# Optimization experiments

Hardware: AMD Instinct MI355X
Metric: run time of the kernel (lower is better)

## Reference

```python
import jax, jax.numpy as jnp
import numpy as np

B, S, D, F, E, CAP = 4, 2048, 1024, 4096, 8, 320


def setup_inputs() -> dict:
    key = jax.random.key(0)
    k1, k2, k3, k4 = jax.random.split(key, 4)
    return {
        "hidden_states": jax.random.normal(k1, (B, S, D), dtype=jnp.float32),
        "router_w": jax.random.normal(k2, (D, E), dtype=jnp.float32) * 0.02,
        "wi": jax.random.normal(k3, (E, D, F), dtype=jnp.float32) * 0.02,
        "wo": jax.random.normal(k4, (E, F, D), dtype=jnp.float32) * 0.02,
    }


def reference(hidden_states, router_w, wi, wo):
    # ---- Router (Switch top-1 with per-sequence expert capacity) ----
    b, s, d = hidden_states.shape
    e = router_w.shape[1]
    logits = hidden_states.astype(jnp.float32) @ router_w          # [B,S,E]
    probs = jax.nn.softmax(logits, axis=-1)                        # [B,S,E]
    expert_idx = jnp.argmax(probs, axis=-1)                        # [B,S]
    onehot = jax.nn.one_hot(expert_idx, e, dtype=jnp.int32)        # [B,S,E]
    priority = jnp.cumsum(onehot, axis=1)                          # cumsum over seq dim (dim=-2)
    keep = onehot * (priority <= CAP).astype(jnp.int32)            # capacity-masked router_mask

    # slot of each token within its chosen expert (0-based)
    slot = jnp.take_along_axis(priority, expert_idx[..., None], axis=-1)[..., 0] - 1  # [B,S]
    valid = slot < CAP                                             # dropped tokens exceed capacity
    slot_sc = jnp.where(valid, slot, CAP)                          # out-of-range -> dropped by scatter

    b_ar = jnp.broadcast_to(jnp.arange(b)[:, None], (b, s))
    s_ar = jnp.broadcast_to(jnp.arange(s)[None, :], (b, s))
    dispatch = jnp.zeros((b, e, CAP), jnp.int32).at[b_ar, expert_idx, slot_sc].set(
        s_ar.astype(jnp.int32), mode="drop")                       # [B,E,CAP] token index per slot
    slot_used = jnp.zeros((b, e, CAP), bool).at[b_ar, expert_idx, slot_sc].set(
        valid, mode="drop")                                        # [B,E,CAP]

    # ---- Dispatch: gather tokens into [B,E,CAP,D] ----
    xg = jax.vmap(lambda xb, ib: xb[ib])(hidden_states, dispatch)  # [B,E,CAP,D]

    # ---- Per-expert dense FFN (grouped GEMM) ----
    hg = jax.nn.relu(jnp.einsum("becd,edf->becf", xg, wi))         # [B,E,CAP,F]
    yg = jnp.einsum("becf,efd->becd", hg, wo)                      # [B,E,CAP,D]

    # ---- Combine: scatter expert outputs back; unrouted tokens keep input ----
    idx_back = jnp.where(slot_used, dispatch, s)                   # out-of-range -> dropped
    next_states = jax.vmap(
        lambda xb, ib, yb: xb.at[ib.reshape(-1)].set(yb.reshape(-1, d), mode="drop")
    )(hidden_states, idx_back, yg)                                 # [B,S,D]

    max_prob = jnp.max(probs, axis=-1, keepdims=True)              # [B,S,1]
    out = max_prob * next_states
    expert_index_out = jnp.argmax(keep, axis=-1)                   # [B,S] (0 for dropped tokens)
    return out, logits, expert_index_out
```

## Files before the change

kernel.cpp:

```cpp
#include <hip/hip_runtime.h>
#include <hip/hip_bf16.h>
#include <stdint.h>

#define B_ 4
#define S_ 2048
#define D_ 1024
#define F_ 4096
#define E_ 8
#define CAP_ 320
#define BS_ (B_*S_)
#define MPE 1280

typedef unsigned short u16;
typedef __attribute__((ext_vector_type(8))) short bf16x8;
typedef __attribute__((ext_vector_type(4))) float f32x4;
typedef __attribute__((ext_vector_type(4))) unsigned short u16x4;

__device__ __forceinline__ u16 f2bf(float f) {
  union { float f; uint32_t u; } v; v.f = f;
  uint32_t r = (v.u + 0x7FFFu + ((v.u >> 16) & 1u)) >> 16;
  return (u16)r;
}

__device__ __forceinline__ void gload16(const void* g, void* l) {
  __builtin_amdgcn_global_load_lds(
      (const __attribute__((address_space(1))) uint32_t*)g,
      (__attribute__((address_space(3))) uint32_t*)l, 16, 0, 0);
}

__global__ __launch_bounds__(256) void router_kernel(
    const float* __restrict__ hs, const float* __restrict__ rw,
    float* __restrict__ out, float* __restrict__ logits,
    float* __restrict__ maxp, int* __restrict__ eidx)
{
  const int wv = threadIdx.x >> 6, l = threadIdx.x & 63;
  const int token = blockIdx.x * 4 + wv;
  const float* row = hs + (size_t)token * D_;
  const float4* rw4 = (const float4*)rw;

  double acc0=0, acc1=0, acc2=0, acc3=0, acc4=0, acc5=0, acc6=0, acc7=0;
  float4 v[4];
#pragma unroll
  for (int j = 0; j < 4; ++j) {
    const int d4 = l + j * 64;
    v[j] = ((const float4*)row)[d4];
#pragma unroll
    for (int c = 0; c < 4; ++c) {
      const int d = d4 * 4 + c;
      const float x = (&v[j].x)[c];
      const float4 w0 = rw4[d * 2];
      const float4 w1 = rw4[d * 2 + 1];
      acc0 += (double)x * (double)w0.x;
      acc1 += (double)x * (double)w0.y;
      acc2 += (double)x * (double)w0.z;
      acc3 += (double)x * (double)w0.w;
      acc4 += (double)x * (double)w1.x;
      acc5 += (double)x * (double)w1.y;
      acc6 += (double)x * (double)w1.z;
      acc7 += (double)x * (double)w1.w;
    }
  }
  double acc[E_] = {acc0, acc1, acc2, acc3, acc4, acc5, acc6, acc7};
#pragma unroll
  for (int e = 0; e < E_; ++e) {
#pragma unroll
    for (int off = 32; off; off >>= 1)
      acc[e] += __shfl_xor(acc[e], off);
  }
  float lg[E_];
#pragma unroll
  for (int e = 0; e < E_; ++e) lg[e] = (float)acc[e];

  float lmax = lg[0]; int am = 0;
#pragma unroll
  for (int e = 1; e < E_; ++e) { if (lg[e] > lmax) { lmax = lg[e]; am = e; } }
  float sum = 0.f;
#pragma unroll
  for (int e = 0; e < E_; ++e) sum += expf(lg[e] - lmax);
  const float mp = 1.0f / sum;

  float* orow = out + (size_t)token * D_;
#pragma unroll
  for (int j = 0; j < 4; ++j) {
    float4 o;
    o.x = v[j].x * mp; o.y = v[j].y * mp; o.z = v[j].z * mp; o.w = v[j].w * mp;
    ((float4*)orow)[l + j * 64] = o;
  }
  if (l == 0) {
#pragma unroll
    for (int e = 0; e < E_; ++e) logits[(size_t)token * E_ + e] = lg[e];
    maxp[token] = mp;
    eidx[token] = am;
  }
}

__global__ __launch_bounds__(256) void scan_kernel(
    const int* __restrict__ eidx, int* __restrict__ tok,
    float* __restrict__ eout)
{
  const int b = blockIdx.x >> 3, e = blockIdx.x & 7;
  __shared__ int wsum[4];
  const int tid = threadIdx.x, wv = tid >> 6, l = tid & 63;
  int base = 0;
  for (int ch = 0; ch < S_ / 256; ++ch) {
    const int s = ch * 256 + tid;
    const bool p = (eidx[b * S_ + s] == e);
    const unsigned long long m = __ballot(p);
    const int lp = __popcll(m & ((1ULL << l) - 1ULL));
    if (l == 0) wsum[wv] = __popcll(m);
    __syncthreads();
    int pre = 0, tot = 0;
#pragma unroll
    for (int w = 0; w < 4; ++w) { if (w < wv) pre += wsum[w]; tot += wsum[w]; }
    if (p) {
      const int rank = base + pre + lp;
      if (rank < CAP_) tok[(b * E_ + e) * CAP_ + rank] = s;
      eout[b * S_ + s] = (rank < CAP_) ? (float)e : 0.0f;
    }
    base += tot;
    __syncthreads();
  }
}

__global__ __launch_bounds__(256) void transpose_kernel(
    const float* __restrict__ W, u16* __restrict__ WT, int K, int N)
{
  __shared__ float tile[32][33];
  const int tiles_k = K >> 5, tiles_n = N >> 5;
  const int e = blockIdx.x / (tiles_k * tiles_n);
  const int r = blockIdx.x % (tiles_k * tiles_n);
  const int k0 = (r / tiles_n) << 5, n0 = (r % tiles_n) << 5;
  const int tx = threadIdx.x & 31, ty = threadIdx.x >> 5;
  const float* We = W + (size_t)e * K * N;
  u16* WTe = WT + (size_t)e * K * N;
#pragma unroll
  for (int i = 0; i < 4; ++i)
    tile[ty + i * 8][tx] = We[(size_t)(k0 + ty + i * 8) * N + (n0 + tx)];
  __syncthreads();
#pragma unroll
  for (int i = 0; i < 4; ++i) {
    const int n = n0 + ty + i * 8, k = k0 + tx;
    WTe[(size_t)n * K + k] = f2bf(tile[tx][ty + i * 8]);
  }
}

__global__ __launch_bounds__(256) void gather_kernel(
    const float* __restrict__ hs, const int* __restrict__ tok,
    u16* __restrict__ Xg)
{
  const int bx = blockIdx.x;
  const int e = bx / MPE, r = bx % MPE;
  const int b = r / CAP_, c = r % CAP_;
  const int t = tok[(b * E_ + e) * CAP_ + c];
  const int d = threadIdx.x * 4;
  u16x4 o;
  if (t >= 0) {
    const float4 vv = *(const float4*)(hs + ((size_t)(b * S_ + t)) * D_ + d);
    o[0] = f2bf(vv.x); o[1] = f2bf(vv.y); o[2] = f2bf(vv.z); o[3] = f2bf(vv.w);
  } else {
    o[0] = 0; o[1] = 0; o[2] = 0; o[3] = 0;
  }
  *(u16x4*)(Xg + (size_t)bx * D_ + d) = o;
}

template<int MODE>
__global__ __launch_bounds__(512, 2) void moe_gemm8(
    const u16* __restrict__ Aall, const u16* __restrict__ Btall,
    u16* __restrict__ hgout, float* __restrict__ out,
    const int* __restrict__ tok, const float* __restrict__ maxp,
    const int K, const int ntn)
{
  __shared__ __align__(16) u16 lds[2][2][2][8192];

  const int nwg = gridDim.x;
  const int cpx = nwg >> 3;
  const int bid = blockIdx.x;
  const int swzb = (bid & 7) * cpx + (bid >> 3);
  const int bpe = 5 * ntn;
  const int e = swzb / bpe, rem = swzb % bpe;
  const int m0 = (rem / ntn) * 256, n0 = (rem % ntn) * 256;
  const int N = ntn * 256;

  const u16* Ae = Aall + (size_t)e * MPE * K;
  const u16* Be = Btall + (size_t)e * N * K;

  const int tid = threadIdx.x;
  const int wv = tid >> 6, l = tid & 63;
  const int wr = wv >> 2, wc = wv & 3;
  const int lr = l & 15, lk = l >> 4;
  const int rswz = ((lr >> 3) & 1) << 4;
  const int gs0 = tid ^ (((tid >> 5) & 1) << 1);
  const size_t goff = (size_t)((gs0 >> 2) & 127) * K + (size_t)((gs0 & 3) * 8);
  const int dwoff = wv * 512;

  const u16* pA0 = Ae + (size_t)m0 * K;
  const u16* pA1 = Ae + (size_t)(m0 + 128) * K;
  const u16* pB0 = Be + (size_t)n0 * K;
  const u16* pB1 = Be + (size_t)(n0 + 128) * K;

  const int NT = K >> 6;

  f32x4 acc[8][4];
#pragma unroll
  for (int i = 0; i < 8; ++i)
#pragma unroll
    for (int j = 0; j < 4; ++j) acc[i][j] = (f32x4){0.f, 0.f, 0.f, 0.f};

  bf16x8 fa[8], fb0[4], fb1[4];

#define LDSH(p, ab, h) (&lds[p][ab][h][0])

#define STAGE(dhalf, rb, tt) do {                                          \
    const u16* s_ = (rb) + goff + (size_t)((tt) * 64);                     \
    gload16(s_,      (dhalf) + dwoff);                                     \
    gload16(s_ + 32, (dhalf) + 4096 + dwoff);                              \
  } while (0)

#define READ_A(msub, p) do {                                               \
    _Pragma("unroll")                                                      \
    for (int mf = 0; mf < 4; ++mf)                                         \
      _Pragma("unroll")                                                    \
      for (int kk = 0; kk < 2; ++kk)                                       \
        fa[mf*2+kk] = *(const bf16x8*)&lds[p][0][wr]                       \
            [(kk*128 + (msub)*64 + mf*16 + lr)*32 + ((lk*8) ^ rswz)];      \
  } while (0)

#define READ_B(nsub, p, fb) do {                                           \
    _Pragma("unroll")                                                      \
    for (int nf = 0; nf < 2; ++nf)                                         \
      _Pragma("unroll")                                                    \
      for (int kk = 0; kk < 2; ++kk)                                       \
        fb[nf*2+kk] = *(const bf16x8*)&lds[p][1][wc>>1]                    \
            [(kk*128 + (wc&1)*64 + (nsub)*32 + nf*16 + lr)*32              \
             + ((lk*8) ^ rswz)];                                           \
  } while (0)

#define MFMA_Q(msub, nsub, fb) do {                                        \
    __builtin_amdgcn_s_setprio(1);                                         \
    _Pragma("unroll")                                                      \
    for (int mf = 0; mf < 4; ++mf)                                         \
      _Pragma("unroll")                                                    \
      for (int nf = 0; nf < 2; ++nf)                                       \
        _Pragma("unroll")                                                  \
        for (int kk = 0; kk < 2; ++kk)                                     \
          acc[(msub)*4+mf][(nsub)*2+nf] =                                  \
              __builtin_amdgcn_mfma_f32_16x16x32_bf16(                     \
                  fa[mf*2+kk], fb[nf*2+kk],                                \
                  acc[(msub)*4+mf][(nsub)*2+nf], 0, 0, 0);                 \
    __builtin_amdgcn_s_setprio(0);                                         \
  } while (0)

#define BAR() __builtin_amdgcn_s_barrier()
#define LGKM0() do { asm volatile("s_waitcnt lgkmcnt(0)" ::: "memory");    \
                     __builtin_amdgcn_sched_barrier(0); } while (0)
#define VM4() asm volatile("s_waitcnt vmcnt(4)" ::: "memory")

#define DO_TILE(p, pn, tA, tB) do {                                        \
                                                                   \
    READ_A(0, p); READ_B(0, p, fb0);                                       \
    STAGE(LDSH(pn, 0, 0), pA0, (tA));                                      \
    BAR(); LGKM0();                                                        \
    MFMA_Q(0, 0, fb0);                                                     \
    BAR();                                                                 \
                                                                   \
    READ_B(1, p, fb1);                                                     \
    STAGE(LDSH(pn, 0, 1), pA1, (tA));                                      \
    BAR(); LGKM0();                                                        \
    MFMA_Q(0, 1, fb1);                                                     \
    BAR();                                                                 \
                                                                   \
    READ_A(1, p);                                                          \
    STAGE(LDSH(p, 1, 0), pB0, (tB));                                       \
    BAR(); LGKM0();                                                        \
    MFMA_Q(1, 0, fb0);                                                     \
    BAR();                                                                 \
                                                                   \
    STAGE(LDSH(p, 1, 1), pB1, (tB));                                       \
    BAR();                                                                 \
    MFMA_Q(1, 1, fb1);                                                     \
    VM4(); BAR();                                                          \
  } while (0)

  STAGE(LDSH(0, 1, 0), pB0, 0);
  STAGE(LDSH(0, 1, 1), pB1, 0);
  STAGE(LDSH(0, 0, 0), pA0, 0);
  STAGE(LDSH(0, 0, 1), pA1, 0);
  STAGE(LDSH(1, 1, 0), pB0, 1);
  STAGE(LDSH(1, 1, 1), pB1, 1);
  VM4(); BAR();

  for (int t = 0; t < NT; t += 2) {
    const int tB0 = (t + 2 < NT) ? t + 2 : t;
    const int tB1 = (t + 3 < NT) ? t + 3 : t + 1;
    DO_TILE(0, 1, t + 1, tB0);
    DO_TILE(1, 0, tB0, tB1);
  }

  if (MODE == 1) {
#pragma unroll
    for (int i = 0; i < 8; ++i) {
#pragma unroll
      for (int r = 0; r < 4; ++r) {
        const int grow = m0 + wr * 128 + i * 16 + lk * 4 + r;
        u16* hrow = hgout + ((size_t)e * MPE + grow) * (size_t)N + n0 + wc * 64;
#pragma unroll
        for (int j = 0; j < 4; ++j)
          hrow[j * 16 + lr] = f2bf(fmaxf(acc[i][j][r], 0.0f));
      }
    }
  } else {
#pragma unroll
    for (int i = 0; i < 8; ++i) {
#pragma unroll
      for (int r = 0; r < 4; ++r) {
        const int grow = m0 + wr * 128 + i * 16 + lk * 4 + r;
        const int b = grow / CAP_, c = grow % CAP_;
        const int t = tok[(b * E_ + e) * CAP_ + c];
        if (t >= 0) {
          const float sc = maxp[b * S_ + t];
          float* orow = out + ((size_t)(b * S_ + t)) * D_ + n0 + wc * 64;
#pragma unroll
          for (int j = 0; j < 4; ++j)
            orow[j * 16 + lr] = sc * acc[i][j][r];
        }
      }
    }
  }
#undef LDSH
#undef STAGE
#undef READ_A
#undef READ_B
#undef MFMA_Q
#undef BAR
#undef LGKM0
#undef VM4
#undef DO_TILE
}

extern "C" void kernel_launch(void* const* d_in, const int* in_sizes, int n_in,
                              void* d_out, int out_size, void* d_ws, size_t ws_size,
                              hipStream_t stream)
{
  const float* hs = (const float*)d_in[0];
  const float* rw = (const float*)d_in[1];
  const float* wi = (const float*)d_in[2];
  const float* wo = (const float*)d_in[3];

  float* out    = (float*)d_out;
  float* logits = out + (size_t)BS_ * D_;
  float* eout   = logits + (size_t)BS_ * E_;

  uint8_t* ws = (uint8_t*)d_ws;
  int*   tok  = (int*)(ws + 0);
  float* maxp = (float*)(ws + 40960);
  int*   eidx = (int*)(ws + 73728);
  u16*   Xg   = (u16*)(ws + 131072);
  u16*   hg   = (u16*)(ws + 21102592);
  u16*   wT   = (u16*)(ws + 104988672);
  if (ws_size < 172097536ULL) return;

  hipMemsetAsync(tok, 0xFF, 40960, stream);

  router_kernel<<<BS_ / 4, 256, 0, stream>>>(hs, rw, out, logits, maxp, eidx);
  scan_kernel<<<B_ * E_, 256, 0, stream>>>(eidx, tok, eout);
  transpose_kernel<<<E_ * (D_ / 32) * (F_ / 32), 256, 0, stream>>>(wi, wT, D_, F_);
  gather_kernel<<<E_ * MPE, 256, 0, stream>>>(hs, tok, Xg);
  moe_gemm8<1><<<E_ * 5 * (F_ / 256), 512, 0, stream>>>(
      Xg, wT, hg, nullptr, tok, maxp, D_, F_ / 256);
  transpose_kernel<<<E_ * (F_ / 32) * (D_ / 32), 256, 0, stream>>>(wo, wT, F_, D_);
  moe_gemm8<2><<<E_ * 5 * (D_ / 256), 512, 0, stream>>>(
      hg, wT, nullptr, out, tok, maxp, F_, D_ / 256);
}
```

Before: 340.3 us.

## Fuse weight transposes into router and GEMM launches, restructure GEMM prefetch pipeline

The wi transpose is merged into the router launch as extra blocks, and when workspace allows, the wo transpose is appended as extra blocks to the first GEMM launch. The transpose is rewritten with bigger 128x64 tiles and 16-byte bf16 stores. The per-token scaling of unrouted outputs moves from the router into the scan, so only dropped tokens are copied, and the memset is replaced by in-kernel initialisation. The GEMM K-loop prefetch order and vmcnt waits are reworked to stage A further ahead. The goal is fewer launches, better transpose bandwidth and overlap, at the cost of more complex scheduling and extra LDS use in the fused paths.

```diff
diff --git a/kernel.cpp b/kernel.cpp
--- a/kernel.cpp
+++ b/kernel.cpp
@@ -15,6 +15,7 @@
 typedef __attribute__((ext_vector_type(8))) short bf16x8;
 typedef __attribute__((ext_vector_type(4))) float f32x4;
 typedef __attribute__((ext_vector_type(4))) unsigned short u16x4;
+typedef __attribute__((ext_vector_type(8))) unsigned short u16x8;
 
 __device__ __forceinline__ u16 f2bf(float f) {
   union { float f; uint32_t u; } v; v.f = f;
@@ -28,26 +29,68 @@
       (__attribute__((address_space(3))) uint32_t*)l, 16, 0, 0);
 }
 
-__global__ __launch_bounds__(256) void router_kernel(
+__device__ __forceinline__ void transpose_block(
+    const float* __restrict__ W, u16* __restrict__ WT,
+    const int K, const int N, const int bid, void* ldsraw)
+{
+  float (*tile)[65] = (float(*)[65])ldsraw;
+  const int tk = K >> 7, tn = N >> 6;
+  const int e = bid / (tk * tn), r = bid % (tk * tn);
+  const int k0 = (r / tn) << 7, n0 = (r % tn) << 6;
+  const float* We = W + (size_t)e * K * N;
+  u16* WTe = WT + (size_t)e * N * K;
+  const int t = threadIdx.x;
+  const int fr = t >> 2, c0 = (t & 3) * 16;
+#pragma unroll
+  for (int j = 0; j < 4; ++j) {
+    const float4 v = *(const float4*)(We + (size_t)(k0 + fr) * N + n0 + c0 + j * 4);
+    tile[fr][c0 + j*4 + 0] = v.x; tile[fr][c0 + j*4 + 1] = v.y;
+    tile[fr][c0 + j*4 + 2] = v.z; tile[fr][c0 + j*4 + 3] = v.w;
+  }
+  __syncthreads();
+  const int nr = t >> 3, kk0 = (t & 7) * 16;
+  u16x8 o0, o1;
+#pragma unroll
+  for (int j = 0; j < 8; ++j) o0[j] = f2bf(tile[kk0 + j][nr]);
+#pragma unroll
+  for (int j = 0; j < 8; ++j) o1[j] = f2bf(tile[kk0 + 8 + j][nr]);
+  u16* dst = WTe + (size_t)(n0 + nr) * K + k0 + kk0;
+  *(u16x8*)dst = o0;
+  *(u16x8*)(dst + 8) = o1;
+}
+
+__global__ __launch_bounds__(512) void transpose_kernel(
+    const float* __restrict__ W, u16* __restrict__ WT, const int K, const int N)
+{
+  __shared__ __align__(16) float tile[128][65];
+  transpose_block(W, WT, K, N, blockIdx.x, (void*)tile);
+}
+
+__global__ __launch_bounds__(512) void prep_kernel(
     const float* __restrict__ hs, const float* __restrict__ rw,
-    float* __restrict__ out, float* __restrict__ logits,
-    float* __restrict__ maxp, int* __restrict__ eidx)
-{
+    const float* __restrict__ wi, u16* __restrict__ wT,
+    float* __restrict__ logits, float* __restrict__ maxp,
+    int* __restrict__ eidx, const int twiT)
+{
+  __shared__ __align__(16) float tile[128][65];
+  if ((int)blockIdx.x < twiT) {
+    transpose_block(wi, wT, D_, F_, blockIdx.x, (void*)tile);
+    return;
+  }
   const int wv = threadIdx.x >> 6, l = threadIdx.x & 63;
-  const int token = blockIdx.x * 4 + wv;
+  const int token = (blockIdx.x - twiT) * 8 + wv;
   const float* row = hs + (size_t)token * D_;
   const float4* rw4 = (const float4*)rw;
 
   double acc0=0, acc1=0, acc2=0, acc3=0, acc4=0, acc5=0, acc6=0, acc7=0;
-  float4 v[4];
 #pragma unroll
   for (int j = 0; j < 4; ++j) {
     const int d4 = l + j * 64;
-    v[j] = ((const float4*)row)[d4];
+    const float4 v = ((const float4*)row)[d4];
 #pragma unroll
     for (int c = 0; c < 4; ++c) {
       const int d = d4 * 4 + c;
-      const float x = (&v[j].x)[c];
+      const float x = (&v.x)[c];
       const float4 w0 = rw4[d * 2];
       const float4 w1 = rw4[d * 2 + 1];
       acc0 += (double)x * (double)w0.x;
@@ -67,40 +110,33 @@
     for (int off = 32; off; off >>= 1)
       acc[e] += __shfl_xor(acc[e], off);
   }
-  float lg[E_];
-#pragma unroll
-  for (int e = 0; e < E_; ++e) lg[e] = (float)acc[e];
-
-  float lmax = lg[0]; int am = 0;
-#pragma unroll
-  for (int e = 1; e < E_; ++e) { if (lg[e] > lmax) { lmax = lg[e]; am = e; } }
-  float sum = 0.f;
-#pragma unroll
-  for (int e = 0; e < E_; ++e) sum += expf(lg[e] - lmax);
-  const float mp = 1.0f / sum;
-
-  float* orow = out + (size_t)token * D_;
-#pragma unroll
-  for (int j = 0; j < 4; ++j) {
-    float4 o;
-    o.x = v[j].x * mp; o.y = v[j].y * mp; o.z = v[j].z * mp; o.w = v[j].w * mp;
-    ((float4*)orow)[l + j * 64] = o;
-  }
   if (l == 0) {
+    float lg[E_];
+#pragma unroll
+    for (int e = 0; e < E_; ++e) lg[e] = (float)acc[e];
+    float lmax = lg[0]; int am = 0;
+#pragma unroll
+    for (int e = 1; e < E_; ++e) { if (lg[e] > lmax) { lmax = lg[e]; am = e; } }
+    float sum = 0.f;
+#pragma unroll
+    for (int e = 0; e < E_; ++e) sum += expf(lg[e] - lmax);
 #pragma unroll
     for (int e = 0; e < E_; ++e) logits[(size_t)token * E_ + e] = lg[e];
-    maxp[token] = mp;
+    maxp[token] = 1.0f / sum;
     eidx[token] = am;
   }
 }
 
 __global__ __launch_bounds__(256) void scan_kernel(
     const int* __restrict__ eidx, int* __restrict__ tok,
-    float* __restrict__ eout)
+    float* __restrict__ eout, const float* __restrict__ hs,
+    const float* __restrict__ maxp, float* __restrict__ out)
 {
   const int b = blockIdx.x >> 3, e = blockIdx.x & 7;
   __shared__ int wsum[4];
   const int tid = threadIdx.x, wv = tid >> 6, l = tid & 63;
+  for (int i = tid; i < CAP_; i += 256) tok[(b * E_ + e) * CAP_ + i] = -1;
+  __syncthreads();
   int base = 0;
   for (int ch = 0; ch < S_ / 256; ++ch) {
     const int s = ch * 256 + tid;
@@ -114,33 +150,23 @@
     for (int w = 0; w < 4; ++w) { if (w < wv) pre += wsum[w]; tot += wsum[w]; }
     if (p) {
       const int rank = base + pre + lp;
-      if (rank < CAP_) tok[(b * E_ + e) * CAP_ + rank] = s;
-      eout[b * S_ + s] = (rank < CAP_) ? (float)e : 0.0f;
+      if (rank < CAP_) {
+        tok[(b * E_ + e) * CAP_ + rank] = s;
+        eout[b * S_ + s] = (float)e;
+      } else {
+        eout[b * S_ + s] = 0.0f;
+        const float mp = maxp[b * S_ + s];
+        const float4* src = (const float4*)(hs + (size_t)(b * S_ + s) * D_);
+        float4* dst = (float4*)(out + (size_t)(b * S_ + s) * D_);
+        for (int j = 0; j < D_ / 4; ++j) {
+          const float4 vv = src[j];
+          float4 o; o.x = vv.x * mp; o.y = vv.y * mp; o.z = vv.z * mp; o.w = vv.w * mp;
+          dst[j] = o;
+        }
+      }
     }
     base += tot;
     __syncthreads();
-  }
-}
-
-__global__ __launch_bounds__(256) void transpose_kernel(
-    const float* __restrict__ W, u16* __restrict__ WT, int K, int N)
-{
-  __shared__ float tile[32][33];
-  const int tiles_k = K >> 5, tiles_n = N >> 5;
-  const int e = blockIdx.x / (tiles_k * tiles_n);
-  const int r = blockIdx.x % (tiles_k * tiles_n);
-  const int k0 = (r / tiles_n) << 5, n0 = (r % tiles_n) << 5;
-  const int tx = threadIdx.x & 31, ty = threadIdx.x >> 5;
-  const float* We = W + (size_t)e * K * N;
-  u16* WTe = WT + (size_t)e * K * N;
-#pragma unroll
-  for (int i = 0; i < 4; ++i)
-    tile[ty + i * 8][tx] = We[(size_t)(k0 + ty + i * 8) * N + (n0 + tx)];
-  __syncthreads();
-#pragma unroll
-  for (int i = 0; i < 4; ++i) {
-    const int n = n0 + ty + i * 8, k = k0 + tx;
-    WTe[(size_t)n * K + k] = f2bf(tile[tx][ty + i * 8]);
   }
 }
 
@@ -168,12 +194,18 @@
     const u16* __restrict__ Aall, const u16* __restrict__ Btall,
     u16* __restrict__ hgout, float* __restrict__ out,
     const int* __restrict__ tok, const float* __restrict__ maxp,
-    const int K, const int ntn)
+    const int K, const int ntn, const int gemm_blocks,
+    const float* __restrict__ Wtr, u16* __restrict__ WTtr,
+    const int tK, const int tN)
 {
   __shared__ __align__(16) u16 lds[2][2][2][8192];
 
-  const int nwg = gridDim.x;
-  const int cpx = nwg >> 3;
+  if ((int)blockIdx.x >= gemm_blocks) {
+    transpose_block(Wtr, WTtr, tK, tN, blockIdx.x - gemm_blocks, (void*)lds);
+    return;
+  }
+
+  const int cpx = gemm_blocks >> 3;
   const int bid = blockIdx.x;
   const int swzb = (bid & 7) * cpx + (bid >> 3);
   const int bpe = 5 * ntn;
@@ -253,47 +285,50 @@
 #define BAR() __builtin_amdgcn_s_barrier()
 #define LGKM0() do { asm volatile("s_waitcnt lgkmcnt(0)" ::: "memory");    \
                      __builtin_amdgcn_sched_barrier(0); } while (0)
-#define VM4() asm volatile("s_waitcnt vmcnt(4)" ::: "memory")
-
-#define DO_TILE(p, pn, tA, tB) do {                                        \
+#define VM6() asm volatile("s_waitcnt vmcnt(6)" ::: "memory")
+#define VM0() asm volatile("s_waitcnt vmcnt(0)" ::: "memory")
+
+#define DO_TILE(p, pn, tc) do {                                            \
                                                                    \
     READ_A(0, p); READ_B(0, p, fb0);                                       \
-    STAGE(LDSH(pn, 0, 0), pA0, (tA));                                      \
+    if ((tc) + 1 < NT) STAGE(LDSH(pn, 0, 1), pA1, (tc) + 1);               \
     BAR(); LGKM0();                                                        \
     MFMA_Q(0, 0, fb0);                                                     \
     BAR();                                                                 \
                                                                    \
     READ_B(1, p, fb1);                                                     \
-    STAGE(LDSH(pn, 0, 1), pA1, (tA));                                      \
     BAR(); LGKM0();                                                        \
     MFMA_Q(0, 1, fb1);                                                     \
     BAR();                                                                 \
                                                                    \
     READ_A(1, p);                                                          \
-    STAGE(LDSH(p, 1, 0), pB0, (tB));                                       \
+    if ((tc) + 2 < NT) STAGE(LDSH(p, 1, 0), pB0, (tc) + 2);                \
     BAR(); LGKM0();                                                        \
     MFMA_Q(1, 0, fb0);                                                     \
     BAR();                                                                 \
                                                                    \
-    STAGE(LDSH(p, 1, 1), pB1, (tB));                                       \
+    if ((tc) + 2 < NT) {                                                   \
+      STAGE(LDSH(p, 1, 1), pB1, (tc) + 2);                                 \
+      STAGE(LDSH(p, 0, 0), pA0, (tc) + 2);                                 \
+    }                                                                      \
     BAR();                                                                 \
     MFMA_Q(1, 1, fb1);                                                     \
-    VM4(); BAR();                                                          \
+    if ((tc) >= NT - 2) VM0(); else VM6();                                 \
+    BAR();                                                                 \
   } while (0)
 
+  STAGE(LDSH(0, 0, 0), pA0, 0);
+  STAGE(LDSH(0, 0, 1), pA1, 0);
   STAGE(LDSH(0, 1, 0), pB0, 0);
   STAGE(LDSH(0, 1, 1), pB1, 0);
-  STAGE(LDSH(0, 0, 0), pA0, 0);
-  STAGE(LDSH(0, 0, 1), pA1, 0);
+  STAGE(LDSH(1, 0, 0), pA0, 1);
   STAGE(LDSH(1, 1, 0), pB0, 1);
   STAGE(LDSH(1, 1, 1), pB1, 1);
-  VM4(); BAR();
+  VM6(); BAR();
 
   for (int t = 0; t < NT; t += 2) {
-    const int tB0 = (t + 2 < NT) ? t + 2 : t;
-    const int tB1 = (t + 3 < NT) ? t + 3 : t + 1;
-    DO_TILE(0, 1, t + 1, tB0);
-    DO_TILE(1, 0, tB0, tB1);
+    DO_TILE(0, 1, t);
+    DO_TILE(1, 0, t + 1);
   }
 
   if (MODE == 1) {
@@ -333,7 +368,8 @@
 #undef MFMA_Q
 #undef BAR
 #undef LGKM0
-#undef VM4
+#undef VM6
+#undef VM0
 #undef DO_TILE
 }
 
@@ -356,18 +392,31 @@
   int*   eidx = (int*)(ws + 73728);
   u16*   Xg   = (u16*)(ws + 131072);
   u16*   hg   = (u16*)(ws + 21102592);
-  u16*   wT   = (u16*)(ws + 104988672);
+  u16*   wiT  = (u16*)(ws + 104988672);
   if (ws_size < 172097536ULL) return;
-
-  hipMemsetAsync(tok, 0xFF, 40960, stream);
-
-  router_kernel<<<BS_ / 4, 256, 0, stream>>>(hs, rw, out, logits, maxp, eidx);
-  scan_kernel<<<B_ * E_, 256, 0, stream>>>(eidx, tok, eout);
-  transpose_kernel<<<E_ * (D_ / 32) * (F_ / 32), 256, 0, stream>>>(wi, wT, D_, F_);
+  const bool big = ws_size >= 239206400ULL;
+  u16* woT = big ? (u16*)(ws + 172097536) : wiT;
+
+  const int twiT = E_ * (D_ / 128) * (F_ / 64);
+  const int twoT = E_ * (F_ / 128) * (D_ / 64);
+  const int g1 = E_ * 5 * (F_ / 256);
+  const int g2 = E_ * 5 * (D_ / 256);
+
+  prep_kernel<<<twiT + BS_ / 8, 512, 0, stream>>>(
+      hs, rw, wi, wiT, logits, maxp, eidx, twiT);
+  scan_kernel<<<B_ * E_, 256, 0, stream>>>(eidx, tok, eout, hs, maxp, out);
   gather_kernel<<<E_ * MPE, 256, 0, stream>>>(hs, tok, Xg);
-  moe_gemm8<1><<<E_ * 5 * (F_ / 256), 512, 0, stream>>>(
-      Xg, wT, hg, nullptr, tok, maxp, D_, F_ / 256);
-  transpose_kernel<<<E_ * (F_ / 32) * (D_ / 32), 256, 0, stream>>>(wo, wT, F_, D_);
-  moe_gemm8<2><<<E_ * 5 * (D_ / 256), 512, 0, stream>>>(
-      hg, wT, nullptr, out, tok, maxp, F_, D_ / 256);
-}
+
+  if (big) {
+    moe_gemm8<1><<<g1 + twoT, 512, 0, stream>>>(
+        Xg, wiT, hg, nullptr, tok, maxp, D_, F_ / 256, g1, wo, woT, F_, D_);
+  } else {
+    moe_gemm8<1><<<g1, 512, 0, stream>>>(
+        Xg, wiT, hg, nullptr, tok, maxp, D_, F_ / 256, g1,
+        nullptr, nullptr, 0, 0);
+    transpose_kernel<<<twoT, 512, 0, stream>>>(wo, woT, F_, D_);
+  }
+  moe_gemm8<2><<<g2, 512, 0, stream>>>(
+      hg, woT, nullptr, out, tok, maxp, F_, D_ / 256, g2,
+      nullptr, nullptr, 0, 0);
+}
```

After: 343.9 us. Within noise of the previous version (+1.1%).
